# Optimization experiments

Hardware: AMD Instinct MI355X
Metric: run time of the kernel (lower is better)

The kernel has to match this reference:

```python
import jax, jax.numpy as jnp
import numpy as np

P, NT = 4, 524288
DZ = 1.0e-3     # z step (m)
DT = 0.01       # time step (ps)
GAMMA = 1.0e-3  # nonlinear coefficient
FR = 0.18       # Raman fraction
OMEGA0 = 1830.0 # carrier angular frequency (rad/ps), ~1030 nm


def setup_inputs() -> dict:
    key = jax.random.key(0)
    ks = jax.random.split(key, 7)
    A_re = jax.random.normal(ks[0], (P, NT), jnp.float32) * 0.5
    A_im = jax.random.normal(ks[1], (P, NT), jnp.float32) * 0.5
    S = jax.random.uniform(ks[2], (P, P, P, P), jnp.float32) * 0.1  # mode overlap tensor
    D_re = jax.random.normal(ks[3], (P, NT), jnp.float32) * 0.1
    D_im = jax.random.normal(ks[4], (P, NT), jnp.float32) * 0.01
    hrw_re = jax.random.normal(ks[5], (NT,), jnp.float32)
    hrw_im = jax.random.normal(ks[6], (NT,), jnp.float32)
    omega = (2.0 * np.pi * np.fft.fftfreq(NT, DT)).astype(np.float32)
    return {"A_re": A_re, "A_im": A_im, "S": S, "D_re": D_re, "D_im": D_im,
            "hrw_re": hrw_re, "hrw_im": hrw_im, "omega": jnp.asarray(omega), "nz": 10}


def _propagate(A0, S, D, hrw, omega, nz):
    # half-step linear (dispersion) phase, applied in the frequency domain
    lin = jnp.exp(0.5j * DZ * D)                       # (P, Nt)
    # self-steepening spectral prefactor  i*gamma*(1 + Omega/omega0)
    pref = (1j * GAMMA) * (1.0 + omega / OMEGA0)       # (Nt,)
    hrw_c = jnp.conj(hrw)                              # (Nt,)

    def nl(A):  # dA/dz from Kerr + Raman + self-steepening, A: (P, Nt) time domain
        S_kerr = jnp.einsum('pqrs,qt,rt,st->pt', S, A, A, jnp.conj(A))
        T = A[:, None, :] * jnp.conj(A)[None, :, :]    # (P, P, Nt)
        T_conv = jnp.fft.ifft(jnp.fft.fft(T, axis=-1) * hrw_c, axis=-1) * DT
        Vpl = jnp.einsum('pmrs,rst->pmt', S, T_conv)   # (P, P, Nt)
        S_raman = jnp.einsum('pmt,mt->pt', Vpl, A)     # (P, Nt)
        S_total = (1.0 - FR) * S_kerr + FR * S_raman
        return jnp.fft.fft(pref * jnp.fft.ifft(S_total, axis=-1), axis=-1)

    def step(carry, _):
        f, fw = carry
        fw = fw * lin
        f = jnp.fft.fft(fw, axis=-1)
        # RK4 for the nonlinear sub-step
        k1 = DZ * nl(f)
        k2 = DZ * nl(f + 0.5 * k1)
        k3 = DZ * nl(f + 0.5 * k2)
        k4 = DZ * nl(f + k3)
        f = f + (k1 + 2.0 * k2 + 2.0 * k3 + k4) / 6.0
        fw = jnp.fft.ifft(f, axis=-1) * lin
        return (f, fw), None

    fw0 = jnp.fft.ifft(A0, axis=-1)
    (f, fw), _ = jax.lax.scan(step, (A0, fw0), None, length=nz)
    return jnp.fft.fft(fw, axis=-1)


def reference(A_re, A_im, S, D_re, D_im, hrw_re, hrw_im, omega, nz):
    A = (A_re + 1j * A_im).astype(jnp.complex64)
    D = (D_re + 1j * D_im).astype(jnp.complex64)
    hrw = (hrw_re + 1j * hrw_im).astype(jnp.complex64)
    out = _propagate(A, S, D, hrw, omega, nz)          # (P, Nt) complex64
    return jnp.stack([out.real, out.imag])             # (2, P, Nt) float32
```

## Files before the change

kernel.cpp:

```cpp
#include <hip/hip_runtime.h>
#include <math.h>

#define NTOT (1 << 19)
#define NN1 512
#define NN2 1024
#define PM 4
#define NZ_STEPS 10

static const float DZv = 1.0e-3f;
static const float DTv = 0.01f;
static const float GAMMAv = 1.0e-3f;
static const float FRv = 0.18f;
static const float OMEGA0v = 1830.0f;

typedef float2 cplx;
__device__ inline cplx cmul(cplx a, cplx b) { return make_float2(a.x * b.x - a.y * b.y, a.x * b.y + a.y * b.x); }
__device__ inline cplx cadd(cplx a, cplx b) { return make_float2(a.x + b.x, a.y + b.y); }
__device__ inline cplx csub(cplx a, cplx b) { return make_float2(a.x - b.x, a.y - b.y); }
__device__ inline cplx cscale(cplx a, float s) { return make_float2(a.x * s, a.y * s); }
__device__ inline cplx conjc(cplx a) { return make_float2(a.x, -a.y); }
__device__ inline cplx expi_pi(float a, float sgn) {
    float s, c;
    sincospif(a, &s, &c);
    return make_float2(c, sgn * s);
}
__device__ inline int dig4rev10(int j) {
    return ((j & 3) << 8) | (((j >> 2) & 3) << 6) | (((j >> 4) & 3) << 4) | (((j >> 6) & 3) << 2) | ((j >> 8) & 3);
}
__device__ inline int b4rev8(int t) {
    return ((t & 3) << 6) | (((t >> 2) & 3) << 4) | (((t >> 4) & 3) << 2) | ((t >> 6) & 3);
}
__device__ inline int islot_512(int k1) { return ((k1 & 1) << 8) | b4rev8(k1 >> 1); }

#define SK(q) ((q) + ((q) >> 4))

#define TW_SZ 596
#define TWOFF(L) ((L) == 4 ? 0 : (L) == 16 ? 4 : (L) == 64 ? 20 : 84)
#define TWR2 340
__device__ inline void init_tw(cplx* tw, int tid) {
    for (int idx = tid; idx < TW_SZ; idx += 256) {
        float a;
        if (idx < 4) a = (float)idx * (0.5f / 4.0f);
        else if (idx < 20) a = (float)(idx - 4) * (0.5f / 16.0f);
        else if (idx < 84) a = (float)(idx - 20) * (0.5f / 64.0f);
        else if (idx < 340) a = (float)(idx - 84) * (0.5f / 256.0f);
        else a = (float)(idx - 340) * (1.0f / 256.0f);
        float s, c;
        sincospif(a, &s, &c);
        tw[idx] = make_float2(c, s);
    }
}
__device__ inline cplx twget(const cplx* tw, int off, int b, float SGN) {
    cplx t = tw[off + b];
    return make_float2(t.x, SGN * t.y);
}

__device__ inline void r4dif_w(cplx& x0, cplx& x1, cplx& x2, cplx& x3, cplx w1, float SGN) {
    cplx t0 = cadd(x0, x2), t1 = cadd(x1, x3), t2 = csub(x0, x2), t3 = csub(x1, x3);
    cplx ct3 = make_float2(-SGN * t3.y, SGN * t3.x);
    cplx w2 = cmul(w1, w1), w3 = cmul(w2, w1);
    x0 = cadd(t0, t1);
    x1 = cmul(cadd(t2, ct3), w1);
    x2 = cmul(csub(t0, t1), w2);
    x3 = cmul(csub(t2, ct3), w3);
}
__device__ inline void r4dif0(cplx& x0, cplx& x1, cplx& x2, cplx& x3, float SGN) {
    cplx t0 = cadd(x0, x2), t1 = cadd(x1, x3), t2 = csub(x0, x2), t3 = csub(x1, x3);
    cplx ct3 = make_float2(-SGN * t3.y, SGN * t3.x);
    x0 = cadd(t0, t1); x1 = cadd(t2, ct3); x2 = csub(t0, t1); x3 = csub(t2, ct3);
}
__device__ inline void r4dit_w(cplx& x0, cplx& x1, cplx& x2, cplx& x3, cplx w1, float SGN) {
    cplx w2 = cmul(w1, w1), w3 = cmul(w2, w1);
    cplx z1 = cmul(x1, w1), z2 = cmul(x2, w2), z3 = cmul(x3, w3);
    cplx t0 = cadd(x0, z2), t1 = cadd(z1, z3), t2 = csub(x0, z2), t3 = csub(z1, z3);
    cplx ct3 = make_float2(-SGN * t3.y, SGN * t3.x);
    x0 = cadd(t0, t1); x1 = cadd(t2, ct3); x2 = csub(t0, t1); x3 = csub(t2, ct3);
}
__device__ inline void r4dit0(cplx& x0, cplx& x1, cplx& x2, cplx& x3, float SGN) {
    cplx t0 = cadd(x0, x2), t1 = cadd(x1, x3), t2 = csub(x0, x2), t3 = csub(x1, x3);
    cplx ct3 = make_float2(-SGN * t3.y, SGN * t3.x);
    x0 = cadd(t0, t1); x1 = cadd(t2, ct3); x2 = csub(t0, t1); x3 = csub(t2, ct3);
}

template <bool INV, bool TFORM>
__global__ __launch_bounds__(256) void kA1(const cplx* __restrict__ in, cplx* __restrict__ out, int pair0) {
    __shared__ cplx ld[1024 + 64];
    __shared__ cplx tw[TW_SZ];
    const float SGN = INV ? 1.0f : -1.0f;
    int row = blockIdx.y;
    int n1 = blockIdx.x;
    int tid = threadIdx.x;
    const cplx* srcA;
    const cplx* srcB = nullptr;
    if (TFORM) {
        int rs = pair0 + row;
        srcA = in + (size_t)(rs >> 2) * NTOT;
        srcB = in + (size_t)(rs & 3) * NTOT;
    } else {
        srcA = in + (size_t)row * NTOT;
    }
    cplx* dst = out + (size_t)row * NTOT;
    size_t base = (size_t)n1 * NN2;
    cplx x0, x1, x2, x3;
    if (TFORM) {
        x0 = cmul(srcA[base + tid], conjc(srcB[base + tid]));
        x1 = cmul(srcA[base + tid + 256], conjc(srcB[base + tid + 256]));
        x2 = cmul(srcA[base + tid + 512], conjc(srcB[base + tid + 512]));
        x3 = cmul(srcA[base + tid + 768], conjc(srcB[base + tid + 768]));
    } else {
        x0 = srcA[base + tid];
        x1 = srcA[base + tid + 256];
        x2 = srcA[base + tid + 512];
        x3 = srcA[base + tid + 768];
    }
    init_tw(tw, tid);
    __syncthreads();
    r4dif_w(x0, x1, x2, x3, twget(tw, 84, tid, SGN), SGN);
    ld[SK(tid)] = x0; ld[SK(tid + 256)] = x1; ld[SK(tid + 512)] = x2; ld[SK(tid + 768)] = x3;
    __syncthreads();
    #pragma unroll
    for (int L = 64; L >= 4; L >>= 2) {
        int b = tid & (L - 1), g = tid / L;
        int p0 = g * 4 * L + b;
        cplx y0 = ld[SK(p0)], y1 = ld[SK(p0 + L)], y2 = ld[SK(p0 + 2 * L)], y3 = ld[SK(p0 + 3 * L)];
        r4dif_w(y0, y1, y2, y3, twget(tw, TWOFF(L), b, SGN), SGN);
        ld[SK(p0)] = y0; ld[SK(p0 + L)] = y1; ld[SK(p0 + 2 * L)] = y2; ld[SK(p0 + 3 * L)] = y3;
        __syncthreads();
    }
    {
        int p0 = 4 * tid;
        cplx y0 = ld[SK(p0)], y1 = ld[SK(p0 + 1)], y2 = ld[SK(p0 + 2)], y3 = ld[SK(p0 + 3)];
        r4dif0(y0, y1, y2, y3, SGN);
        int c = dig4rev10(p0);
        cplx w = expi_pi((float)(n1 * c) * (2.0f / (float)NTOT), SGN);
        if (INV) w = cscale(w, 1.0f / (float)NTOT);
        cplx dlt = expi_pi((float)n1 * (1.0f / 1024.0f), SGN);
        cplx o0 = cmul(y0, w);
        w = cmul(w, dlt);
        cplx o1 = cmul(y1, w);
        w = cmul(w, dlt);
        cplx o2 = cmul(y2, w);
        w = cmul(w, dlt);
        cplx o3 = cmul(y3, w);
        float4* d4 = (float4*)(dst + base + p0);
        d4[0] = make_float4(o0.x, o0.y, o1.x, o1.y);
        d4[1] = make_float4(o2.x, o2.y, o3.x, o3.y);
    }
}

template <bool CONV, int TMODE>
__global__ __launch_bounds__(256) void kM(const cplx* in, cplx* out, const cplx* __restrict__ tab) {
    __shared__ cplx ld[8 * 545];
    __shared__ cplx tw[TW_SZ];
    const float SGN_F = CONV ? -1.0f : 1.0f;
    const float SGN_B = -SGN_F;
    int row = blockIdx.y;
    int jb = blockIdx.x * 8;
    const cplx* src = in + (size_t)row * NTOT;
    cplx* dst = out + (size_t)row * NTOT;
    const cplx* trow = (TMODE == 3) ? tab : tab + (size_t)row * NTOT;
    int tid = threadIdx.x;
    int jj = tid & 7, n10 = tid >> 3;
    cplx v[16];
    #pragma unroll
    for (int m = 0; m < 16; m++) v[m] = src[(size_t)(n10 + 32 * m) * NN2 + jb + jj];
    init_tw(tw, tid);
    __syncthreads();
    #pragma unroll
    for (int m = 0; m < 8; m++) {
        int b = n10 + 32 * m;
        cplx u = v[m], w = v[m + 8];
        v[m] = cadd(u, w);
        v[m + 8] = cmul(csub(u, w), twget(tw, TWR2, b, SGN_F));
    }
    #pragma unroll
    for (int m = 0; m < 8; m++) {
        int b = n10 + 32 * m;
        ld[jj * 545 + SK(b)] = v[m];
        ld[jj * 545 + SK(b + 256)] = v[m + 8];
    }
    __syncthreads();
    #pragma unroll
    for (int L = 64; L >= 4; L >>= 2) {
        #pragma unroll
        for (int it = 0; it < 4; it++) {
            int gbf = it * 256 + tid;
            int r = gbf >> 7, rr = gbf & 127;
            int h = rr >> 6, s = rr & 63;
            int b = s & (L - 1), g = s / L;
            int q0 = h * 256 + g * 4 * L + b;
            cplx* rp = ld + r * 545;
            cplx y0 = rp[SK(q0)], y1 = rp[SK(q0 + L)], y2 = rp[SK(q0 + 2 * L)], y3 = rp[SK(q0 + 3 * L)];
            r4dif_w(y0, y1, y2, y3, twget(tw, TWOFF(L), b, SGN_F), SGN_F);
            rp[SK(q0)] = y0; rp[SK(q0 + L)] = y1; rp[SK(q0 + 2 * L)] = y2; rp[SK(q0 + 3 * L)] = y3;
        }
        __syncthreads();
    }
    #pragma unroll
    for (int it = 0; it < 4; it++) {
        int gbf = it * 256 + tid;
        int r = gbf >> 7, rr = gbf & 127;
        int h = rr >> 6, s = rr & 63;
        int q0 = h * 256 + 4 * s;
        cplx* rp = ld + r * 545;
        cplx y0 = rp[SK(q0)], y1 = rp[SK(q0 + 1)], y2 = rp[SK(q0 + 2)], y3 = rp[SK(q0 + 3)];
        r4dif0(y0, y1, y2, y3, SGN_F);
        size_t tb = (size_t)(jb + r) * NN1 + q0;
        const cplx* tp = trow + tb;
        cplx t0 = tp[0], t1 = tp[1], t2 = tp[2], t3 = tp[3];
        if (TMODE == 2) { t0 = cmul(t0, t0); t1 = cmul(t1, t1); t2 = cmul(t2, t2); t3 = cmul(t3, t3); }
        y0 = cmul(y0, t0); y1 = cmul(y1, t1); y2 = cmul(y2, t2); y3 = cmul(y3, t3);
        r4dit0(y0, y1, y2, y3, SGN_B);
        rp[SK(q0)] = y0; rp[SK(q0 + 1)] = y1; rp[SK(q0 + 2)] = y2; rp[SK(q0 + 3)] = y3;
    }
    __syncthreads();
    #pragma unroll
    for (int L = 4; L <= 64; L <<= 2) {
        #pragma unroll
        for (int it = 0; it < 4; it++) {
            int gbf = it * 256 + tid;
            int r = gbf >> 7, rr = gbf & 127;
            int h = rr >> 6, s = rr & 63;
            int b = s & (L - 1), g = s / L;
            int q0 = h * 256 + g * 4 * L + b;
            cplx* rp = ld + r * 545;
            cplx y0 = rp[SK(q0)], y1 = rp[SK(q0 + L)], y2 = rp[SK(q0 + 2 * L)], y3 = rp[SK(q0 + 3 * L)];
            r4dit_w(y0, y1, y2, y3, twget(tw, TWOFF(L), b, SGN_B), SGN_B);
            rp[SK(q0)] = y0; rp[SK(q0 + L)] = y1; rp[SK(q0 + 2 * L)] = y2; rp[SK(q0 + 3 * L)] = y3;
        }
        __syncthreads();
    }
    #pragma unroll
    for (int it = 0; it < 8; it++) {
        int f = it, b = tid;
        cplx* rp = ld + f * 545;
        cplx u = rp[SK(b)], w = rp[SK(b + 256)];
        cplx wv = cmul(w, twget(tw, TWR2, b, SGN_B));
        cplx o0 = cadd(u, wv), o1 = csub(u, wv);
        int j = jb + f;
        int k2 = dig4rev10(j);
        cplx cbase = expi_pi((float)(b * k2) * (2.0f / (float)NTOT), SGN_B);
        if (CONV) cbase = cscale(cbase, 1.0f / (float)NTOT);
        cplx eps = expi_pi((float)k2 * (1.0f / 1024.0f), SGN_B);
        o0 = cmul(o0, cbase);
        o1 = cmul(o1, cmul(cbase, eps));
        dst[(size_t)j * NN1 + b] = o0;
        dst[(size_t)j * NN1 + b + 256] = o1;
    }
}

template <bool INV, bool RKEPI, int TN1>
__global__ __launch_bounds__(256) void kB2(const cplx* __restrict__ in, cplx* __restrict__ out,
                                           cplx* __restrict__ fP, cplx* __restrict__ kaccP,
                                           cplx* __restrict__ AtmpP, int stage) {
    __shared__ cplx ld[TN1 * 1091];
    __shared__ cplx tw[TW_SZ];
    const float SGN = INV ? 1.0f : -1.0f;
    int row = blockIdx.y;
    int n1b = blockIdx.x * TN1;
    const cplx* src = in + (size_t)row * NTOT;
    int tid = threadIdx.x;
    constexpr int NQ = TN1 / 2;
    constexpr int JR = 256 / NQ;
    int qi = tid & (NQ - 1), jr = tid / NQ;
    const float4* s4 = (const float4*)src;
    #pragma unroll
    for (int m = 0; m < 1024 / JR; m++) {
        int j = jr + JR * m;
        float4 v = s4[(size_t)j * (NN1 / 2) + (n1b / 2) + qi];
        ld[(2 * qi) * 1091 + SK(j)] = make_float2(v.x, v.y);
        ld[(2 * qi + 1) * 1091 + SK(j)] = make_float2(v.z, v.w);
    }
    init_tw(tw, tid);
    __syncthreads();
    #pragma unroll
    for (int it = 0; it < TN1; it++) {
        int bfid = it * 256 + tid;
        int r = bfid >> 8, s = bfid & 255;
        int q0 = 4 * s;
        cplx* rp = ld + r * 1091;
        cplx y0 = rp[SK(q0)], y1 = rp[SK(q0 + 1)], y2 = rp[SK(q0 + 2)], y3 = rp[SK(q0 + 3)];
        r4dit0(y0, y1, y2, y3, SGN);
        rp[SK(q0)] = y0; rp[SK(q0 + 1)] = y1; rp[SK(q0 + 2)] = y2; rp[SK(q0 + 3)] = y3;
    }
    __syncthreads();
    #pragma unroll
    for (int L = 4; L <= 64; L <<= 2) {
        #pragma unroll
        for (int it = 0; it < TN1; it++) {
            int bfid = it * 256 + tid;
            int r = bfid >> 8, s = bfid & 255;
            int b = s & (L - 1), g = s / L;
            int q0 = g * 4 * L + b;
            cplx* rp = ld + r * 1091;
            cplx y0 = rp[SK(q0)], y1 = rp[SK(q0 + L)], y2 = rp[SK(q0 + 2 * L)], y3 = rp[SK(q0 + 3 * L)];
            r4dit_w(y0, y1, y2, y3, twget(tw, TWOFF(L), b, SGN), SGN);
            rp[SK(q0)] = y0; rp[SK(q0 + L)] = y1; rp[SK(q0 + 2 * L)] = y2; rp[SK(q0 + 3 * L)] = y3;
        }
        __syncthreads();
    }
    #pragma unroll
    for (int it = 0; it < TN1; it++) {
        int bfid = it * 256 + tid;
        int r = bfid >> 8, b = bfid & 255;
        cplx* rp = ld + r * 1091;
        cplx y0 = rp[SK(b)], y1 = rp[SK(b + 256)], y2 = rp[SK(b + 512)], y3 = rp[SK(b + 768)];
        r4dit_w(y0, y1, y2, y3, twget(tw, 84, b, SGN), SGN);
        cplx ya[4] = {y0, y1, y2, y3};
        size_t tbase = (size_t)(n1b + r) * NN2 + b;
        #pragma unroll
        for (int q = 0; q < 4; q++) {
            size_t off = (size_t)row * NTOT + tbase + q * 256;
            cplx v = ya[q];
            if (RKEPI) {
                if (stage == 1) {
                    kaccP[off] = v;
                    AtmpP[off] = cadd(fP[off], cscale(v, 0.5f));
                } else if (stage == 2) {
                    kaccP[off] = cadd(kaccP[off], cscale(v, 2.0f));
                    AtmpP[off] = cadd(fP[off], cscale(v, 0.5f));
                } else if (stage == 3) {
                    kaccP[off] = cadd(kaccP[off], cscale(v, 2.0f));
                    AtmpP[off] = cadd(fP[off], v);
                } else {
                    fP[off] = cadd(fP[off], cscale(cadd(kaccP[off], v), 1.0f / 6.0f));
                }
            } else {
                out[off] = v;
            }
        }
    }
}

__global__ __launch_bounds__(256) void k_tables(const float* __restrict__ D_re, const float* __restrict__ D_im,
                                                const float* __restrict__ hrw_re, const float* __restrict__ hrw_im,
                                                const float* __restrict__ omega,
                                                cplx* __restrict__ lin, cplx* __restrict__ pref, cplx* __restrict__ hrwc) {
    int k = blockIdx.x * 256 + threadIdx.x;
    if (k >= NTOT) return;
    int k2 = k & (NN2 - 1), k1 = k >> 10;
    int j = dig4rev10(k2), i = islot_512(k1);
    int s2 = j * NN1 + i;
    float om = omega[k];
    pref[s2] = make_float2(0.0f, GAMMAv * DZv * (1.0f + om / OMEGA0v));
    hrwc[s2] = make_float2(hrw_re[k] * DTv, -hrw_im[k] * DTv);
    for (int p = 0; p < PM; p++) {
        float dr = D_re[(size_t)p * NTOT + k], di = D_im[(size_t)p * NTOT + k];
        float amp = expf(-0.5f * DZv * di);
        float s, c;
        sincosf(0.5f * DZv * dr, &s, &c);
        lin[(size_t)p * NTOT + s2] = make_float2(amp * c, amp * s);
    }
}

__global__ void k_in(const float* __restrict__ Are, const float* __restrict__ Aim, cplx* __restrict__ f) {
    __shared__ cplx t[32][33];
    int p = blockIdx.z;
    int n1b = blockIdx.x * 32, n2b = blockIdx.y * 32;
    int tx = threadIdx.x, ty = threadIdx.y;
    const float* ar = Are + (size_t)p * NTOT;
    const float* ai = Aim + (size_t)p * NTOT;
    for (int yy = ty; yy < 32; yy += 8) {
        size_t idx = (size_t)(n2b + yy) * NN1 + (n1b + tx);
        t[yy][tx] = make_float2(ar[idx], ai[idx]);
    }
    __syncthreads();
    cplx* dst = f + (size_t)p * NTOT;
    for (int yy = ty; yy < 32; yy += 8) {
        dst[(size_t)(n1b + yy) * NN2 + (n2b + tx)] = t[tx][yy];
    }
}

__global__ void k_out(const cplx* __restrict__ fin, float* __restrict__ out) {
    __shared__ cplx t[32][33];
    int p = blockIdx.z;
    int n1b = blockIdx.x * 32, n2b = blockIdx.y * 32;
    int tx = threadIdx.x, ty = threadIdx.y;
    const cplx* src = fin + (size_t)p * NTOT;
    for (int yy = ty; yy < 32; yy += 8) {
        t[yy][tx] = src[(size_t)(n1b + yy) * NN2 + (n2b + tx)];
    }
    __syncthreads();
    float* outr = out + (size_t)p * NTOT;
    float* outi = out + (size_t)(PM + p) * NTOT;
    for (int yy = ty; yy < 32; yy += 8) {
        cplx v = t[tx][yy];
        size_t idx = (size_t)(n2b + yy) * NN1 + (n1b + tx);
        outr[idx] = v.x;
        outi[idx] = v.y;
    }
}

template <bool KERR>
__global__ __launch_bounds__(256) void k_ram(const cplx* __restrict__ Tc, const cplx* __restrict__ A,
                                             const float* __restrict__ S, cplx* __restrict__ St,
                                             int pair0, int nrows) {
    __shared__ float Ssh[256];
    int tid = threadIdx.x;
    Ssh[tid] = S[tid];
    __syncthreads();
    size_t pos = (size_t)blockIdx.x * 256 + tid;
    cplx a[4];
    for (int m = 0; m < 4; m++) a[m] = A[(size_t)m * NTOT + pos];
    cplx acc[4];
    for (int p = 0; p < 4; p++) acc[p] = make_float2(0.f, 0.f);
    for (int rowi = 0; rowi < nrows; rowi++) {
        int rs = pair0 + rowi, r = rs >> 2, s = rs & 3;
        cplx tc = Tc[(size_t)rowi * NTOT + pos];
        for (int p = 0; p < 4; p++) {
            cplx c = make_float2(0.f, 0.f);
            for (int m = 0; m < 4; m++) {
                float coef = Ssh[((p * 4 + m) * 4 + r) * 4 + s];
                c.x += coef * a[m].x;
                c.y += coef * a[m].y;
            }
            acc[p] = cadd(acc[p], cmul(c, tc));
        }
    }
    if (KERR) {
        cplx pp[4][4];
        for (int r = 0; r < 4; r++)
            for (int s = 0; s < 4; s++) pp[r][s] = cmul(a[r], conjc(a[s]));
        for (int p = 0; p < 4; p++) {
            cplx kacc = make_float2(0.f, 0.f);
            for (int q = 0; q < 4; q++) {
                cplx g = make_float2(0.f, 0.f);
                for (int r = 0; r < 4; r++)
                    for (int s = 0; s < 4; s++) {
                        float coef = Ssh[((p * 4 + q) * 4 + r) * 4 + s];
                        g.x += coef * pp[r][s].x;
                        g.y += coef * pp[r][s].y;
                    }
                kacc = cadd(kacc, cmul(g, a[q]));
            }
            St[(size_t)p * NTOT + pos] = cadd(cscale(kacc, 1.0f - FRv), cscale(acc[p], FRv));
        }
    } else {
        for (int p = 0; p < 4; p++) {
            size_t idx = (size_t)p * NTOT + pos;
            St[idx] = cadd(St[idx], cscale(acc[p], FRv));
        }
    }
}

extern "C" void kernel_launch(void* const* d_in, const int* in_sizes, int n_in,
                              void* d_out, int out_size, void* d_ws, size_t ws_size,
                              hipStream_t stream) {
    const float* Are = (const float*)d_in[0];
    const float* Aim = (const float*)d_in[1];
    const float* S = (const float*)d_in[2];
    const float* Dre = (const float*)d_in[3];
    const float* Dim = (const float*)d_in[4];
    const float* hre = (const float*)d_in[5];
    const float* him = (const float*)d_in[6];
    const float* omega = (const float*)d_in[7];

    const size_t ROW = (size_t)NTOT;
    const bool big = ws_size >= 50ULL * ROW * sizeof(cplx);
    if (!big && ws_size < 38ULL * ROW * sizeof(cplx)) return;

    cplx *f, *Atmp, *kacc, *St, *Z, *Tb, *lin, *pref, *hrwc;
    cplx* basep = (cplx*)d_ws;
    if (big) {
        f = basep;            Atmp = f + 4 * ROW;   kacc = Atmp + 4 * ROW;
        lin = kacc + 4 * ROW; pref = lin + 4 * ROW; hrwc = pref + ROW;
        Z = hrwc + ROW;       Tb = Z + 16 * ROW;    St = Z;
    } else {
        f = basep;            Atmp = f + 4 * ROW;   kacc = Atmp + 4 * ROW;
        St = kacc + 4 * ROW;  Z = St + 4 * ROW;     Tb = Z + 8 * ROW;
        lin = Tb + 8 * ROW;   pref = lin + 4 * ROW; hrwc = pref + ROW;
    }

    dim3 b256(256);
    dim3 gT(16, 32, 4), bT(32, 8);
    dim3 gPW1(NTOT / 256);

    k_tables<<<gPW1, b256, 0, stream>>>(Dre, Dim, hre, him, omega, lin, pref, hrwc);
    k_in<<<gT, bT, 0, stream>>>(Are, Aim, f);

    for (int step = 0; step < NZ_STEPS; step++) {
        kA1<true, false><<<dim3(512, 4), b256, 0, stream>>>(f, Z, 0);
        if (step == 0)
            kM<false, 1><<<dim3(128, 4), b256, 0, stream>>>(Z, Z, lin);
        else
            kM<false, 2><<<dim3(128, 4), b256, 0, stream>>>(Z, Z, lin);
        kB2<false, false, 4><<<dim3(128, 4), b256, 0, stream>>>(Z, f, nullptr, nullptr, nullptr, 0);
        for (int st = 1; st <= 4; st++) {
            const cplx* Aarg = (st == 1) ? f : Atmp;
            if (big) {
                kA1<false, true><<<dim3(512, 16), b256, 0, stream>>>(Aarg, Z, 0);
                kM<true, 3><<<dim3(128, 16), b256, 0, stream>>>(Z, Z, hrwc);
                kB2<true, false, 8><<<dim3(64, 16), b256, 0, stream>>>(Z, Tb, nullptr, nullptr, nullptr, 0);
                k_ram<true><<<gPW1, b256, 0, stream>>>(Tb, Aarg, S, St, 0, 16);
                kA1<true, false><<<dim3(512, 4), b256, 0, stream>>>(St, Tb, 0);
                kM<false, 3><<<dim3(128, 4), b256, 0, stream>>>(Tb, Tb, pref);
                kB2<false, true, 4><<<dim3(128, 4), b256, 0, stream>>>(Tb, nullptr, f, kacc, Atmp, st);
            } else {
                for (int bb = 0; bb < 2; bb++) {
                    kA1<false, true><<<dim3(512, 8), b256, 0, stream>>>(Aarg, Z, bb * 8);
                    kM<true, 3><<<dim3(128, 8), b256, 0, stream>>>(Z, Z, hrwc);
                    kB2<true, false, 8><<<dim3(64, 8), b256, 0, stream>>>(Z, Tb, nullptr, nullptr, nullptr, 0);
                    if (bb == 0)
                        k_ram<true><<<gPW1, b256, 0, stream>>>(Tb, Aarg, S, St, 0, 8);
                    else
                        k_ram<false><<<gPW1, b256, 0, stream>>>(Tb, Aarg, S, St, 8, 8);
                }
                kA1<true, false><<<dim3(512, 4), b256, 0, stream>>>(St, Z, 0);
                kM<false, 3><<<dim3(128, 4), b256, 0, stream>>>(Z, Z, pref);
                kB2<false, true, 4><<<dim3(128, 4), b256, 0, stream>>>(Z, nullptr, f, kacc, Atmp, st);
            }
        }
    }
    kA1<true, false><<<dim3(512, 4), b256, 0, stream>>>(f, Z, 0);
    kM<false, 1><<<dim3(128, 4), b256, 0, stream>>>(Z, Z, lin);
    kB2<false, false, 4><<<dim3(128, 4), b256, 0, stream>>>(Z, Atmp, nullptr, nullptr, nullptr, 0);
    k_out<<<gT, bT, 0, stream>>>(Atmp, (float*)d_out);
}
```

Measured before the change: 9.198 ms.

## Transpose middle FFT output and fuse final inverse FFT pass with Raman contraction

The middle FFT kernel now writes its output transposed, n1-major with contiguous float4 stores, so the final FFT pass reads one contiguous 1024-point row per block. A new kernel fuses the last inverse-FFT pass of all 16 Raman correlation rows with the S-tensor contraction and Kerr term, so the 16-row convolution buffer is never written to or reread from global memory. The workspace layout is simplified to a single configuration. In exchange, the fused kernel loops over 16 rows serially per block with a barrier for each FFT stage, and runs only 512 blocks, which lowers parallelism.

```diff
diff --git a/kernel.cpp b/kernel.cpp
--- a/kernel.cpp
+++ b/kernel.cpp
@@ -148,6 +148,23 @@
     }
 }
 
+#define APPLY_CT(o, n1v)                                                        \
+    {                                                                           \
+        cplx W0 = expi_pi((float)((n1v) * k2b) * (2.0f / (float)NTOT), SGN_B);  \
+        if (CONV) W0 = cscale(W0, 1.0f / (float)NTOT);                          \
+        cplx P1 = expi_pi((float)(n1v) * (1.0f / 1024.0f), SGN_B);              \
+        cplx P2 = expi_pi((float)(n1v) * (1.0f / 4096.0f), SGN_B);              \
+        cplx wct = W0;                                                          \
+        o[0] = cmul(o[0], wct);                                                 \
+        wct = cmul(wct, P1); o[1] = cmul(o[1], wct);                            \
+        wct = cmul(wct, P1); o[2] = cmul(o[2], wct);                            \
+        wct = cmul(wct, P1); o[3] = cmul(o[3], wct);                            \
+        wct = cmul(W0, P2);  o[4] = cmul(o[4], wct);                            \
+        wct = cmul(wct, P1); o[5] = cmul(o[5], wct);                            \
+        wct = cmul(wct, P1); o[6] = cmul(o[6], wct);                            \
+        wct = cmul(wct, P1); o[7] = cmul(o[7], wct);                            \
+    }
+
 template <bool CONV, int TMODE>
 __global__ __launch_bounds__(256) void kM(const cplx* in, cplx* out, const cplx* __restrict__ tab) {
     __shared__ cplx ld[8 * 545];
@@ -230,87 +247,71 @@
         }
         __syncthreads();
     }
-    #pragma unroll
-    for (int it = 0; it < 8; it++) {
-        int f = it, b = tid;
-        cplx* rp = ld + f * 545;
-        cplx u = rp[SK(b)], w = rp[SK(b + 256)];
-        cplx wv = cmul(w, twget(tw, TWR2, b, SGN_B));
-        cplx o0 = cadd(u, wv), o1 = csub(u, wv);
-        int j = jb + f;
-        int k2 = dig4rev10(j);
-        cplx cbase = expi_pi((float)(b * k2) * (2.0f / (float)NTOT), SGN_B);
-        if (CONV) cbase = cscale(cbase, 1.0f / (float)NTOT);
-        cplx eps = expi_pi((float)k2 * (1.0f / 1024.0f), SGN_B);
-        o0 = cmul(o0, cbase);
-        o1 = cmul(o1, cmul(cbase, eps));
-        dst[(size_t)j * NN1 + b] = o0;
-        dst[(size_t)j * NN1 + b + 256] = o1;
-    }
-}
-
-template <bool INV, bool RKEPI, int TN1>
-__global__ __launch_bounds__(256) void kB2(const cplx* __restrict__ in, cplx* __restrict__ out,
-                                           cplx* __restrict__ fP, cplx* __restrict__ kaccP,
-                                           cplx* __restrict__ AtmpP, int stage) {
-    __shared__ cplx ld[TN1 * 1091];
+    {
+        int t = tid;
+        cplx r2 = twget(tw, TWR2, t, SGN_B);
+        cplx oa[8], ob[8];
+        #pragma unroll
+        for (int f = 0; f < 8; f++) {
+            cplx u = ld[f * 545 + SK(t)];
+            cplx w = ld[f * 545 + SK(t + 256)];
+            cplx wv = cmul(w, r2);
+            oa[f] = cadd(u, wv);
+            ob[f] = csub(u, wv);
+        }
+        int k2b = dig4rev10(jb);
+        APPLY_CT(oa, t);
+        APPLY_CT(ob, t + 256);
+        float4* da = (float4*)(dst + (size_t)t * NN2 + jb);
+        da[0] = make_float4(oa[0].x, oa[0].y, oa[1].x, oa[1].y);
+        da[1] = make_float4(oa[2].x, oa[2].y, oa[3].x, oa[3].y);
+        da[2] = make_float4(oa[4].x, oa[4].y, oa[5].x, oa[5].y);
+        da[3] = make_float4(oa[6].x, oa[6].y, oa[7].x, oa[7].y);
+        float4* db = (float4*)(dst + (size_t)(t + 256) * NN2 + jb);
+        db[0] = make_float4(ob[0].x, ob[0].y, ob[1].x, ob[1].y);
+        db[1] = make_float4(ob[2].x, ob[2].y, ob[3].x, ob[3].y);
+        db[2] = make_float4(ob[4].x, ob[4].y, ob[5].x, ob[5].y);
+        db[3] = make_float4(ob[6].x, ob[6].y, ob[7].x, ob[7].y);
+    }
+}
+
+template <bool RKEPI>
+__global__ __launch_bounds__(256) void kB2T(const cplx* __restrict__ in, cplx* __restrict__ out,
+                                            cplx* __restrict__ fP, cplx* __restrict__ kaccP,
+                                            cplx* __restrict__ AtmpP, int stage) {
+    __shared__ cplx ld[1024 + 64];
     __shared__ cplx tw[TW_SZ];
-    const float SGN = INV ? 1.0f : -1.0f;
+    const float SGN = -1.0f;
     int row = blockIdx.y;
-    int n1b = blockIdx.x * TN1;
-    const cplx* src = in + (size_t)row * NTOT;
+    int n1 = blockIdx.x;
     int tid = threadIdx.x;
-    constexpr int NQ = TN1 / 2;
-    constexpr int JR = 256 / NQ;
-    int qi = tid & (NQ - 1), jr = tid / NQ;
-    const float4* s4 = (const float4*)src;
-    #pragma unroll
-    for (int m = 0; m < 1024 / JR; m++) {
-        int j = jr + JR * m;
-        float4 v = s4[(size_t)j * (NN1 / 2) + (n1b / 2) + qi];
-        ld[(2 * qi) * 1091 + SK(j)] = make_float2(v.x, v.y);
-        ld[(2 * qi + 1) * 1091 + SK(j)] = make_float2(v.z, v.w);
-    }
+    size_t base = (size_t)row * NTOT + (size_t)n1 * NN2;
+    const float4* s4 = (const float4*)(in + base);
+    float4 va = s4[2 * tid], vb = s4[2 * tid + 1];
     init_tw(tw, tid);
-    __syncthreads();
-    #pragma unroll
-    for (int it = 0; it < TN1; it++) {
-        int bfid = it * 256 + tid;
-        int r = bfid >> 8, s = bfid & 255;
-        int q0 = 4 * s;
-        cplx* rp = ld + r * 1091;
-        cplx y0 = rp[SK(q0)], y1 = rp[SK(q0 + 1)], y2 = rp[SK(q0 + 2)], y3 = rp[SK(q0 + 3)];
-        r4dit0(y0, y1, y2, y3, SGN);
-        rp[SK(q0)] = y0; rp[SK(q0 + 1)] = y1; rp[SK(q0 + 2)] = y2; rp[SK(q0 + 3)] = y3;
-    }
+    cplx y0 = make_float2(va.x, va.y), y1 = make_float2(va.z, va.w);
+    cplx y2 = make_float2(vb.x, vb.y), y3 = make_float2(vb.z, vb.w);
+    r4dit0(y0, y1, y2, y3, SGN);
+    int q0 = 4 * tid;
+    ld[SK(q0)] = y0; ld[SK(q0 + 1)] = y1; ld[SK(q0 + 2)] = y2; ld[SK(q0 + 3)] = y3;
     __syncthreads();
     #pragma unroll
     for (int L = 4; L <= 64; L <<= 2) {
-        #pragma unroll
-        for (int it = 0; it < TN1; it++) {
-            int bfid = it * 256 + tid;
-            int r = bfid >> 8, s = bfid & 255;
-            int b = s & (L - 1), g = s / L;
-            int q0 = g * 4 * L + b;
-            cplx* rp = ld + r * 1091;
-            cplx y0 = rp[SK(q0)], y1 = rp[SK(q0 + L)], y2 = rp[SK(q0 + 2 * L)], y3 = rp[SK(q0 + 3 * L)];
-            r4dit_w(y0, y1, y2, y3, twget(tw, TWOFF(L), b, SGN), SGN);
-            rp[SK(q0)] = y0; rp[SK(q0 + L)] = y1; rp[SK(q0 + 2 * L)] = y2; rp[SK(q0 + 3 * L)] = y3;
-        }
+        int b = tid & (L - 1), g = tid / L;
+        int p0 = g * 4 * L + b;
+        cplx z0 = ld[SK(p0)], z1 = ld[SK(p0 + L)], z2 = ld[SK(p0 + 2 * L)], z3 = ld[SK(p0 + 3 * L)];
+        r4dit_w(z0, z1, z2, z3, twget(tw, TWOFF(L), b, SGN), SGN);
+        ld[SK(p0)] = z0; ld[SK(p0 + L)] = z1; ld[SK(p0 + 2 * L)] = z2; ld[SK(p0 + 3 * L)] = z3;
         __syncthreads();
     }
-    #pragma unroll
-    for (int it = 0; it < TN1; it++) {
-        int bfid = it * 256 + tid;
-        int r = bfid >> 8, b = bfid & 255;
-        cplx* rp = ld + r * 1091;
-        cplx y0 = rp[SK(b)], y1 = rp[SK(b + 256)], y2 = rp[SK(b + 512)], y3 = rp[SK(b + 768)];
-        r4dit_w(y0, y1, y2, y3, twget(tw, 84, b, SGN), SGN);
-        cplx ya[4] = {y0, y1, y2, y3};
-        size_t tbase = (size_t)(n1b + r) * NN2 + b;
+    {
+        int b = tid;
+        cplx z0 = ld[SK(b)], z1 = ld[SK(b + 256)], z2 = ld[SK(b + 512)], z3 = ld[SK(b + 768)];
+        r4dit_w(z0, z1, z2, z3, twget(tw, 84, b, SGN), SGN);
+        cplx ya[4] = {z0, z1, z2, z3};
         #pragma unroll
         for (int q = 0; q < 4; q++) {
-            size_t off = (size_t)row * NTOT + tbase + q * 256;
+            size_t off = base + b + q * 256;
             cplx v = ya[q];
             if (RKEPI) {
                 if (stage == 1) {
@@ -327,6 +328,110 @@
                 }
             } else {
                 out[off] = v;
+            }
+        }
+    }
+}
+
+template <int NR, bool KERR>
+__global__ __launch_bounds__(256) void kB2R(const cplx* in, const cplx* __restrict__ A,
+                                            const float* __restrict__ Sg, cplx* St, int pair0) {
+    __shared__ cplx ld[1024 + 64];
+    __shared__ cplx tw[TW_SZ];
+    __shared__ float Ssh[256];
+    const float SGN = 1.0f;
+    int n1 = blockIdx.x;
+    int tid = threadIdx.x;
+    Ssh[tid] = Sg[tid];
+    init_tw(tw, tid);
+    size_t tb = (size_t)n1 * NN2 + tid;
+    cplx am[4][4];
+    #pragma unroll
+    for (int m = 0; m < 4; m++)
+        #pragma unroll
+        for (int q = 0; q < 4; q++)
+            am[m][q] = A[(size_t)m * NTOT + tb + q * 256];
+    cplx acc[4][4];
+    #pragma unroll
+    for (int p = 0; p < 4; p++)
+        #pragma unroll
+        for (int q = 0; q < 4; q++) acc[p][q] = make_float2(0.f, 0.f);
+    const float4* s4 = (const float4*)(in + (size_t)n1 * NN2);
+    float4 va = s4[2 * tid], vb = s4[2 * tid + 1];
+    for (int rowi = 0; rowi < NR; rowi++) {
+        cplx y0 = make_float2(va.x, va.y), y1 = make_float2(va.z, va.w);
+        cplx y2 = make_float2(vb.x, vb.y), y3 = make_float2(vb.z, vb.w);
+        int nr = (rowi + 1 < NR) ? rowi + 1 : NR - 1;
+        const float4* s4n = (const float4*)(in + (size_t)nr * NTOT + (size_t)n1 * NN2);
+        va = s4n[2 * tid]; vb = s4n[2 * tid + 1];
+        r4dit0(y0, y1, y2, y3, SGN);
+        int q0 = 4 * tid;
+        ld[SK(q0)] = y0; ld[SK(q0 + 1)] = y1; ld[SK(q0 + 2)] = y2; ld[SK(q0 + 3)] = y3;
+        __syncthreads();
+        #pragma unroll
+        for (int L = 4; L <= 64; L <<= 2) {
+            int b = tid & (L - 1), g = tid / L;
+            int p0 = g * 4 * L + b;
+            cplx z0 = ld[SK(p0)], z1 = ld[SK(p0 + L)], z2 = ld[SK(p0 + 2 * L)], z3 = ld[SK(p0 + 3 * L)];
+            r4dit_w(z0, z1, z2, z3, twget(tw, TWOFF(L), b, SGN), SGN);
+            ld[SK(p0)] = z0; ld[SK(p0 + L)] = z1; ld[SK(p0 + 2 * L)] = z2; ld[SK(p0 + 3 * L)] = z3;
+            __syncthreads();
+        }
+        {
+            int b = tid;
+            cplx z0 = ld[SK(b)], z1 = ld[SK(b + 256)], z2 = ld[SK(b + 512)], z3 = ld[SK(b + 768)];
+            r4dit_w(z0, z1, z2, z3, twget(tw, 84, b, SGN), SGN);
+            cplx tc[4] = {z0, z1, z2, z3};
+            int rs = pair0 + rowi, r = rs >> 2, s = rs & 3;
+            #pragma unroll
+            for (int p = 0; p < 4; p++) {
+                float c0 = Ssh[((p * 4 + 0) * 4 + r) * 4 + s];
+                float c1 = Ssh[((p * 4 + 1) * 4 + r) * 4 + s];
+                float c2 = Ssh[((p * 4 + 2) * 4 + r) * 4 + s];
+                float c3 = Ssh[((p * 4 + 3) * 4 + r) * 4 + s];
+                #pragma unroll
+                for (int q = 0; q < 4; q++) {
+                    cplx c;
+                    c.x = c0 * am[0][q].x + c1 * am[1][q].x + c2 * am[2][q].x + c3 * am[3][q].x;
+                    c.y = c0 * am[0][q].y + c1 * am[1][q].y + c2 * am[2][q].y + c3 * am[3][q].y;
+                    acc[p][q] = cadd(acc[p][q], cmul(c, tc[q]));
+                }
+            }
+        }
+        __syncthreads();
+    }
+    #pragma unroll
+    for (int q = 0; q < 4; q++) {
+        size_t off = tb + q * 256;
+        if (KERR) {
+            cplx pp[4][4];
+            #pragma unroll
+            for (int r = 0; r < 4; r++)
+                #pragma unroll
+                for (int s = 0; s < 4; s++) pp[r][s] = cmul(am[r][q], conjc(am[s][q]));
+            #pragma unroll
+            for (int p = 0; p < 4; p++) {
+                cplx kc = make_float2(0.f, 0.f);
+                #pragma unroll
+                for (int m = 0; m < 4; m++) {
+                    cplx g = make_float2(0.f, 0.f);
+                    #pragma unroll
+                    for (int r = 0; r < 4; r++)
+                        #pragma unroll
+                        for (int s = 0; s < 4; s++) {
+                            float coef = Ssh[((p * 4 + m) * 4 + r) * 4 + s];
+                            g.x += coef * pp[r][s].x;
+                            g.y += coef * pp[r][s].y;
+                        }
+                    kc = cadd(kc, cmul(g, am[m][q]));
+                }
+                St[(size_t)p * NTOT + off] = cadd(cscale(kc, 1.0f - FRv), cscale(acc[p][q], FRv));
+            }
+        } else {
+            #pragma unroll
+            for (int p = 0; p < 4; p++) {
+                size_t idx = (size_t)p * NTOT + off;
+                St[idx] = cadd(St[idx], cscale(acc[p][q], FRv));
             }
         }
     }
@@ -391,58 +496,6 @@
     }
 }
 
-template <bool KERR>
-__global__ __launch_bounds__(256) void k_ram(const cplx* __restrict__ Tc, const cplx* __restrict__ A,
-                                             const float* __restrict__ S, cplx* __restrict__ St,
-                                             int pair0, int nrows) {
-    __shared__ float Ssh[256];
-    int tid = threadIdx.x;
-    Ssh[tid] = S[tid];
-    __syncthreads();
-    size_t pos = (size_t)blockIdx.x * 256 + tid;
-    cplx a[4];
-    for (int m = 0; m < 4; m++) a[m] = A[(size_t)m * NTOT + pos];
-    cplx acc[4];
-    for (int p = 0; p < 4; p++) acc[p] = make_float2(0.f, 0.f);
-    for (int rowi = 0; rowi < nrows; rowi++) {
-        int rs = pair0 + rowi, r = rs >> 2, s = rs & 3;
-        cplx tc = Tc[(size_t)rowi * NTOT + pos];
-        for (int p = 0; p < 4; p++) {
-            cplx c = make_float2(0.f, 0.f);
-            for (int m = 0; m < 4; m++) {
-                float coef = Ssh[((p * 4 + m) * 4 + r) * 4 + s];
-                c.x += coef * a[m].x;
-                c.y += coef * a[m].y;
-            }
-            acc[p] = cadd(acc[p], cmul(c, tc));
-        }
-    }
-    if (KERR) {
-        cplx pp[4][4];
-        for (int r = 0; r < 4; r++)
-            for (int s = 0; s < 4; s++) pp[r][s] = cmul(a[r], conjc(a[s]));
-        for (int p = 0; p < 4; p++) {
-            cplx kacc = make_float2(0.f, 0.f);
-            for (int q = 0; q < 4; q++) {
-                cplx g = make_float2(0.f, 0.f);
-                for (int r = 0; r < 4; r++)
-                    for (int s = 0; s < 4; s++) {
-                        float coef = Ssh[((p * 4 + q) * 4 + r) * 4 + s];
-                        g.x += coef * pp[r][s].x;
-                        g.y += coef * pp[r][s].y;
-                    }
-                kacc = cadd(kacc, cmul(g, a[q]));
-            }
-            St[(size_t)p * NTOT + pos] = cadd(cscale(kacc, 1.0f - FRv), cscale(acc[p], FRv));
-        }
-    } else {
-        for (int p = 0; p < 4; p++) {
-            size_t idx = (size_t)p * NTOT + pos;
-            St[idx] = cadd(St[idx], cscale(acc[p], FRv));
-        }
-    }
-}
-
 extern "C" void kernel_launch(void* const* d_in, const int* in_sizes, int n_in,
                               void* d_out, int out_size, void* d_ws, size_t ws_size,
                               hipStream_t stream) {
@@ -456,20 +509,16 @@
     const float* omega = (const float*)d_in[7];
 
     const size_t ROW = (size_t)NTOT;
-    const bool big = ws_size >= 50ULL * ROW * sizeof(cplx);
-    if (!big && ws_size < 38ULL * ROW * sizeof(cplx)) return;
-
-    cplx *f, *Atmp, *kacc, *St, *Z, *Tb, *lin, *pref, *hrwc;
-    cplx* basep = (cplx*)d_ws;
-    if (big) {
-        f = basep;            Atmp = f + 4 * ROW;   kacc = Atmp + 4 * ROW;
-        lin = kacc + 4 * ROW; pref = lin + 4 * ROW; hrwc = pref + ROW;
-        Z = hrwc + ROW;       Tb = Z + 16 * ROW;    St = Z;
-    } else {
-        f = basep;            Atmp = f + 4 * ROW;   kacc = Atmp + 4 * ROW;
-        St = kacc + 4 * ROW;  Z = St + 4 * ROW;     Tb = Z + 8 * ROW;
-        lin = Tb + 8 * ROW;   pref = lin + 4 * ROW; hrwc = pref + ROW;
-    }
+    if (ws_size < 38ULL * ROW * sizeof(cplx)) return;
+    cplx* f = (cplx*)d_ws;
+    cplx* Atmp = f + 4 * ROW;
+    cplx* kacc = Atmp + 4 * ROW;
+    cplx* lin = kacc + 4 * ROW;
+    cplx* pref = lin + 4 * ROW;
+    cplx* hrwc = pref + 1 * ROW;
+    cplx* Tb = hrwc + 1 * ROW;
+    cplx* Z = Tb + 4 * ROW;
+    cplx* St = Z;
 
     dim3 b256(256);
     dim3 gT(16, 32, 4), bT(32, 8);
@@ -484,35 +533,19 @@
             kM<false, 1><<<dim3(128, 4), b256, 0, stream>>>(Z, Z, lin);
         else
             kM<false, 2><<<dim3(128, 4), b256, 0, stream>>>(Z, Z, lin);
-        kB2<false, false, 4><<<dim3(128, 4), b256, 0, stream>>>(Z, f, nullptr, nullptr, nullptr, 0);
+        kB2T<false><<<dim3(512, 4), b256, 0, stream>>>(Z, f, nullptr, nullptr, nullptr, 0);
         for (int st = 1; st <= 4; st++) {
             const cplx* Aarg = (st == 1) ? f : Atmp;
-            if (big) {
-                kA1<false, true><<<dim3(512, 16), b256, 0, stream>>>(Aarg, Z, 0);
-                kM<true, 3><<<dim3(128, 16), b256, 0, stream>>>(Z, Z, hrwc);
-                kB2<true, false, 8><<<dim3(64, 16), b256, 0, stream>>>(Z, Tb, nullptr, nullptr, nullptr, 0);
-                k_ram<true><<<gPW1, b256, 0, stream>>>(Tb, Aarg, S, St, 0, 16);
-                kA1<true, false><<<dim3(512, 4), b256, 0, stream>>>(St, Tb, 0);
-                kM<false, 3><<<dim3(128, 4), b256, 0, stream>>>(Tb, Tb, pref);
-                kB2<false, true, 4><<<dim3(128, 4), b256, 0, stream>>>(Tb, nullptr, f, kacc, Atmp, st);
-            } else {
-                for (int bb = 0; bb < 2; bb++) {
-                    kA1<false, true><<<dim3(512, 8), b256, 0, stream>>>(Aarg, Z, bb * 8);
-                    kM<true, 3><<<dim3(128, 8), b256, 0, stream>>>(Z, Z, hrwc);
-                    kB2<true, false, 8><<<dim3(64, 8), b256, 0, stream>>>(Z, Tb, nullptr, nullptr, nullptr, 0);
-                    if (bb == 0)
-                        k_ram<true><<<gPW1, b256, 0, stream>>>(Tb, Aarg, S, St, 0, 8);
-                    else
-                        k_ram<false><<<gPW1, b256, 0, stream>>>(Tb, Aarg, S, St, 8, 8);
-                }
-                kA1<true, false><<<dim3(512, 4), b256, 0, stream>>>(St, Z, 0);
-                kM<false, 3><<<dim3(128, 4), b256, 0, stream>>>(Z, Z, pref);
-                kB2<false, true, 4><<<dim3(128, 4), b256, 0, stream>>>(Z, nullptr, f, kacc, Atmp, st);
-            }
+            kA1<false, true><<<dim3(512, 16), b256, 0, stream>>>(Aarg, Z, 0);
+            kM<true, 3><<<dim3(128, 16), b256, 0, stream>>>(Z, Z, hrwc);
+            kB2R<16, true><<<dim3(512), b256, 0, stream>>>(Z, Aarg, S, St, 0);
+            kA1<true, false><<<dim3(512, 4), b256, 0, stream>>>(St, Tb, 0);
+            kM<false, 3><<<dim3(128, 4), b256, 0, stream>>>(Tb, Tb, pref);
+            kB2T<true><<<dim3(512, 4), b256, 0, stream>>>(Tb, nullptr, f, kacc, Atmp, st);
         }
     }
     kA1<true, false><<<dim3(512, 4), b256, 0, stream>>>(f, Z, 0);
     kM<false, 1><<<dim3(128, 4), b256, 0, stream>>>(Z, Z, lin);
-    kB2<false, false, 4><<<dim3(128, 4), b256, 0, stream>>>(Z, Atmp, nullptr, nullptr, nullptr, 0);
+    kB2T<false><<<dim3(512, 4), b256, 0, stream>>>(Z, Atmp, nullptr, nullptr, nullptr, 0);
     k_out<<<gT, bT, 0, stream>>>(Atmp, (float*)d_out);
 }
```

Result: faster. 8.932 ms (-2.9%).
